# Optimization experiments

Measured on AMD Instinct MI355X. Metric: run time of the kernel, lower is better.

## Reference

```python
import jax, jax.numpy as jnp
import numpy as np

TEMPERATURE = 8.0  # sqrt(d_attn) with d_attn = 64
EPS = 1e-12


def _cv_softmax(z):
    """Complex softmax: softmax applied to magnitude, phase preserved.
    result = softmax(|z|, axis=-1) * z / |z|
    """
    mag = jnp.abs(z)                          # [B,H,S,S] real
    w = jax.nn.softmax(mag, axis=-1)          # softmax over magnitudes
    phase = z / jnp.maximum(mag, EPS)         # unit-modulus phase, guarded at 0
    return (w * phase).astype(z.dtype)


def setup_inputs() -> dict:
    key = jax.random.key(0)
    ks = jax.random.split(key, 6)
    shape = (4, 8, 2048, 64)  # [B, H, S, D]
    names = ["q_real", "q_imag", "k_real", "k_imag", "v_real", "v_imag"]
    return {n: jax.random.normal(k, shape, dtype=jnp.float32) for n, k in zip(names, ks)}


def reference(q_real, q_imag, k_real, k_imag, v_real, v_imag):
    q = jax.lax.complex(q_real, q_imag)
    k = jax.lax.complex(k_real, k_imag)
    v = jax.lax.complex(v_real, v_imag)
    # attn = (Q / t) K^T   (complex matmul)   [B,H,S,S]
    attn = jnp.einsum("bhsd,bhtd->bhst", q / TEMPERATURE, k)
    attn = _cv_softmax(attn)  # dropout is identity in eval mode
    out = jnp.einsum("bhst,bhtd->bhsd", attn, v)  # [B,H,S,D] complex
    # return as stacked real array [2, B, H, S, D] (real, imag)
    return jnp.stack([jnp.real(out), jnp.imag(out)], axis=0)
```

## Files before the change

### kernel.cpp

```cpp
#include <hip/hip_runtime.h>
#include <math.h>

typedef _Float16 half8   __attribute__((ext_vector_type(8)));
typedef _Float16 half4_t __attribute__((ext_vector_type(4)));
typedef float    floatx4 __attribute__((ext_vector_type(4)));

namespace {

constexpr int S  = 2048;
constexpr int D  = 64;
constexpr int BH = 32;
constexpr int QT = 64;
constexpr int KT = 64;
constexpr int STP = 72;
constexpr float INV_T = 0.125f;
constexpr size_t PLANE = (size_t)BH * S * D;
constexpr float MBIAS = 2.772588722239781f;

#define MFMA16(a, b, c) __builtin_amdgcn_mfma_f32_16x16x32_f16((a), (b), (c), 0, 0, 0)

typedef __attribute__((address_space(1))) const unsigned int guint;
typedef __attribute__((address_space(3))) unsigned int luint;

__device__ __forceinline__ void gl_lds16(const _Float16* g, _Float16* l) {
    __builtin_amdgcn_global_load_lds((guint*)g, (luint*)l, 16, 0, 0);
}

__global__ __launch_bounds__(256)
void prep_k(const float* __restrict__ kr, const float* __restrict__ ki,
            _Float16* __restrict__ okr, _Float16* __restrict__ oki)
{
    const float* src = blockIdx.z ? ki : kr;
    _Float16*    dst = blockIdx.z ? oki : okr;
    const int bh = (int)blockIdx.y, t0 = (int)blockIdx.x * 64;
    const int r  = (int)threadIdx.x >> 2, cg = (int)threadIdx.x & 3;
    const size_t in = ((size_t)bh * S + t0 + r) * D + cg * 16;
    float4 f0 = *(const float4*)(src + in);
    float4 f1 = *(const float4*)(src + in + 4);
    float4 f2 = *(const float4*)(src + in + 8);
    float4 f3 = *(const float4*)(src + in + 12);
    half8 h0, h1;
    h0[0]=(_Float16)f0.x; h0[1]=(_Float16)f0.y; h0[2]=(_Float16)f0.z; h0[3]=(_Float16)f0.w;
    h0[4]=(_Float16)f1.x; h0[5]=(_Float16)f1.y; h0[6]=(_Float16)f1.z; h0[7]=(_Float16)f1.w;
    h1[0]=(_Float16)f2.x; h1[1]=(_Float16)f2.y; h1[2]=(_Float16)f2.z; h1[3]=(_Float16)f2.w;
    h1[4]=(_Float16)f3.x; h1[5]=(_Float16)f3.y; h1[6]=(_Float16)f3.z; h1[7]=(_Float16)f3.w;
    const int key = r & 7;
    const size_t ob = ((size_t)bh * S + t0 + r) * D;
    *(half8*)(dst + ob + ((cg*2    ) ^ key) * 8) = h0;
    *(half8*)(dst + ob + ((cg*2 + 1) ^ key) * 8) = h1;
}

__global__ __launch_bounds__(256)
void prep_v(const float* __restrict__ vr, const float* __restrict__ vi,
            _Float16* __restrict__ ovr, _Float16* __restrict__ ovi)
{
    __shared__ _Float16 tile[64][72];
    const float* src = blockIdx.z ? vi : vr;
    _Float16*    dst = blockIdx.z ? ovi : ovr;
    const int bh = (int)blockIdx.y, t0 = (int)blockIdx.x * 64;
    const int r  = (int)threadIdx.x >> 2, cg = (int)threadIdx.x & 3;
    const size_t in = ((size_t)bh * S + t0 + r) * D + cg * 16;
    #pragma unroll
    for (int j = 0; j < 4; ++j) {
        float4 f = *(const float4*)(src + in + j * 4);
        tile[cg*16 + j*4 + 0][r] = (_Float16)f.x;
        tile[cg*16 + j*4 + 1][r] = (_Float16)f.y;
        tile[cg*16 + j*4 + 2][r] = (_Float16)f.z;
        tile[cg*16 + j*4 + 3][r] = (_Float16)f.w;
    }
    __syncthreads();
    const int d = r;
    const int key = d & 7;
    const size_t ob = ((size_t)bh * D + d) * S + t0;
    half8 a = *(const half8*)&tile[d][cg*16];
    half8 b = *(const half8*)&tile[d][cg*16 + 8];
    *(half8*)(dst + ob + ((cg*2    ) ^ key) * 8) = a;
    *(half8*)(dst + ob + ((cg*2 + 1) ^ key) * 8) = b;
}

__global__ __launch_bounds__(256, 3)
void cv_attn_f16(const float* __restrict__ qr_g, const float* __restrict__ qi_g,
                 const _Float16* __restrict__ kh_r, const _Float16* __restrict__ kh_i,
                 const _Float16* __restrict__ vt_r, const _Float16* __restrict__ vt_i,
                 float* __restrict__ out)
{
    __shared__ __align__(16) _Float16 sm[4*64*64 + 4*2*16*STP];
    _Float16* const Kr = sm;
    _Float16* const Ki = Kr + 64*64;
    _Float16* const Vr = Ki + 64*64;
    _Float16* const Vi = Vr + 64*64;
    _Float16* const Pb = Vi + 64*64;

    const int tid = (int)threadIdx.x, lane = tid & 63, wv = tid >> 6;
    const int g = lane >> 4, m = lane & 15;

    const int b   = (int)blockIdx.x;
    const int xcd = b & 7, y = b >> 3;
    const int qt  = y & 31, bh = xcd + 8 * (y >> 5);
    const int q0  = qt * QT;
    const size_t base = (size_t)bh * S * D;

    _Float16* const Pr = Pb + wv * (2*16*STP);
    _Float16* const Pi = Pr + 16*STP;

    const int ck0 = ((g    ) ^ (m & 7)) * 8;
    const int ck1 = ((g + 4) ^ (m & 7)) * 8;
    const int rb  = m * 64;
    const int pofs = m * STP + g * 8;

    half8 aqr[2], aqi[2], aqin[2];
    {
        const size_t qoff = base + (size_t)(q0 + wv*16 + m) * D + g*8;
        #pragma unroll
        for (int kc = 0; kc < 2; ++kc) {
            float4 r0 = *(const float4*)(qr_g + qoff + kc*32);
            float4 r1 = *(const float4*)(qr_g + qoff + kc*32 + 4);
            float4 i0 = *(const float4*)(qi_g + qoff + kc*32);
            float4 i1 = *(const float4*)(qi_g + qoff + kc*32 + 4);
            half8 hr, hi;
            hr[0]=(_Float16)(r0.x*INV_T); hr[1]=(_Float16)(r0.y*INV_T);
            hr[2]=(_Float16)(r0.z*INV_T); hr[3]=(_Float16)(r0.w*INV_T);
            hr[4]=(_Float16)(r1.x*INV_T); hr[5]=(_Float16)(r1.y*INV_T);
            hr[6]=(_Float16)(r1.z*INV_T); hr[7]=(_Float16)(r1.w*INV_T);
            hi[0]=(_Float16)(i0.x*INV_T); hi[1]=(_Float16)(i0.y*INV_T);
            hi[2]=(_Float16)(i0.z*INV_T); hi[3]=(_Float16)(i0.w*INV_T);
            hi[4]=(_Float16)(i1.x*INV_T); hi[5]=(_Float16)(i1.y*INV_T);
            hi[6]=(_Float16)(i1.z*INV_T); hi[7]=(_Float16)(i1.w*INV_T);
            aqr[kc] = hr; aqi[kc] = hi; aqin[kc] = -hi;
        }
    }

    floatx4 Or[4], Oi[4];
    float l_run[4] = {0.f, 0.f, 0.f, 0.f};
    #pragma unroll
    for (int nt = 0; nt < 4; ++nt) {
        Or[nt] = (floatx4){0.f,0.f,0.f,0.f};
        Oi[nt] = (floatx4){0.f,0.f,0.f,0.f};
    }

    for (int kt = 0; kt < S/KT; ++kt) {
        const int k0 = kt * KT;
        __syncthreads();

        if (wv < 2) {
            const _Float16* src = (wv ? kh_i : kh_r) + ((size_t)bh*S + k0)*D + lane*8;
            _Float16* dst = (wv ? Ki : Kr);
            #pragma unroll
            for (int i = 0; i < 8; ++i)
                gl_lds16(src + i*512, dst + i*512);
        } else {
            const _Float16* src = (wv == 2 ? vt_r : vt_i)
                                + ((size_t)bh*D + (lane>>3))*S + k0 + (lane&7)*8;
            _Float16* dst = (wv == 2 ? Vr : Vi);
            #pragma unroll
            for (int i = 0; i < 8; ++i)
                gl_lds16(src + (size_t)i*8*S, dst + i*512);
        }
        __syncthreads();

        floatx4 Zr[4], Zi[4];
        #pragma unroll
        for (int nt = 0; nt < 4; ++nt) {
            const int o = nt*16*64 + rb;
            half8 bkr0 = *(const half8*)&Kr[o + ck0];
            half8 bki0 = *(const half8*)&Ki[o + ck0];
            half8 bkr1 = *(const half8*)&Kr[o + ck1];
            half8 bki1 = *(const half8*)&Ki[o + ck1];
            floatx4 zr = (floatx4){0.f,0.f,0.f,0.f};
            floatx4 zi = (floatx4){0.f,0.f,0.f,0.f};
            zr = MFMA16(aqr[0],  bkr0, zr);
            zr = MFMA16(aqin[0], bki0, zr);
            zr = MFMA16(aqr[1],  bkr1, zr);
            zr = MFMA16(aqin[1], bki1, zr);
            zi = MFMA16(aqr[0],  bki0, zi);
            zi = MFMA16(aqi[0],  bkr0, zi);
            zi = MFMA16(aqr[1],  bki1, zi);
            zi = MFMA16(aqi[1],  bkr1, zi);
            Zr[nt] = zr; Zi[nt] = zi;
        }

        #pragma unroll
        for (int nt = 0; nt < 4; ++nt) {
            #pragma unroll
            for (int r = 0; r < 4; ++r) {
                const float zr = Zr[nt][r], zi = Zi[nt][r];
                const float s2  = fmaf(zr, zr, fmaf(zi, zi, 1e-24f));
                const float inv = __builtin_amdgcn_rsqf(s2);
                const float mag = s2 * inv;
                const float p   = __expf(mag - MBIAS);
                l_run[r] += p;
                const float w = p * inv;
                Pr[(4*g + r)*STP + nt*16 + m] = (_Float16)(w * zr);
                Pi[(4*g + r)*STP + nt*16 + m] = (_Float16)(w * zi);
            }
        }

        half8 apr[2], api[2], apin[2];
        apr[0] = *(const half8*)&Pr[pofs];      apr[1] = *(const half8*)&Pr[pofs + 32];
        api[0] = *(const half8*)&Pi[pofs];      api[1] = *(const half8*)&Pi[pofs + 32];
        apin[0] = -api[0]; apin[1] = -api[1];
        #pragma unroll
        for (int nt = 0; nt < 4; ++nt) {
            const int o = nt*16*64 + rb;
            half8 bvr0 = *(const half8*)&Vr[o + ck0];
            half8 bvi0 = *(const half8*)&Vi[o + ck0];
            half8 bvr1 = *(const half8*)&Vr[o + ck1];
            half8 bvi1 = *(const half8*)&Vi[o + ck1];
            floatx4 or_ = Or[nt], oi_ = Oi[nt];
            or_ = MFMA16(apr[0],  bvr0, or_);
            or_ = MFMA16(apin[0], bvi0, or_);
            or_ = MFMA16(apr[1],  bvr1, or_);
            or_ = MFMA16(apin[1], bvi1, or_);
            oi_ = MFMA16(apr[0],  bvi0, oi_);
            oi_ = MFMA16(api[0],  bvr0, oi_);
            oi_ = MFMA16(apr[1],  bvi1, oi_);
            oi_ = MFMA16(api[1],  bvr1, oi_);
            Or[nt] = or_; Oi[nt] = oi_;
        }
    }

    #pragma unroll
    for (int off = 1; off < 16; off <<= 1)
        #pragma unroll
        for (int r = 0; r < 4; ++r)
            l_run[r] += __shfl_xor(l_run[r], off, 64);

    #pragma unroll
    for (int r = 0; r < 4; ++r) {
        const float linv = 1.0f / l_run[r];
        const size_t o = base + (size_t)(q0 + wv*16 + 4*g + r) * D + m;
        #pragma unroll
        for (int nt = 0; nt < 4; ++nt) {
            out[o + nt*16]         = Or[nt][r] * linv;
            out[PLANE + o + nt*16] = Oi[nt][r] * linv;
        }
    }
}

constexpr int ST2 = 72;
__global__ __launch_bounds__(256, 2)
void cv_attn_mfma(const float* __restrict__ qr_g, const float* __restrict__ qi_g,
                  const float* __restrict__ kr_g, const float* __restrict__ ki_g,
                  const float* __restrict__ vr_g, const float* __restrict__ vi_g,
                  float* __restrict__ out)
{
    __shared__ __align__(16) _Float16 sm[4*64*ST2 + 4*2*16*ST2];
    _Float16* const Kr = sm;
    _Float16* const Ki = Kr + 64*ST2;
    _Float16* const Vr = Ki + 64*ST2;
    _Float16* const Vi = Vr + 64*ST2;
    _Float16* const Pb = Vi + 64*ST2;

    const int tid = (int)threadIdx.x, lane = tid & 63, wv = tid >> 6;
    const int g = lane >> 4, m = lane & 15;
    const int bh = (int)blockIdx.y;
    const int q0 = (int)blockIdx.x * QT;
    const size_t base = (size_t)bh * S * D;
    _Float16* const Pr = Pb + wv * (2*16*ST2);
    _Float16* const Pi = Pr + 16*ST2;
    const int lofs = m*ST2 + g*8;

    half8 aqr[2], aqi[2], aqin[2];
    {
        const size_t qoff = base + (size_t)(q0 + wv*16 + m) * D + g*8;
        #pragma unroll
        for (int kc = 0; kc < 2; ++kc) {
            float4 r0 = *(const float4*)(qr_g + qoff + kc*32);
            float4 r1 = *(const float4*)(qr_g + qoff + kc*32 + 4);
            float4 i0 = *(const float4*)(qi_g + qoff + kc*32);
            float4 i1 = *(const float4*)(qi_g + qoff + kc*32 + 4);
            half8 hr, hi;
            hr[0]=(_Float16)(r0.x*INV_T); hr[1]=(_Float16)(r0.y*INV_T);
            hr[2]=(_Float16)(r0.z*INV_T); hr[3]=(_Float16)(r0.w*INV_T);
            hr[4]=(_Float16)(r1.x*INV_T); hr[5]=(_Float16)(r1.y*INV_T);
            hr[6]=(_Float16)(r1.z*INV_T); hr[7]=(_Float16)(r1.w*INV_T);
            hi[0]=(_Float16)(i0.x*INV_T); hi[1]=(_Float16)(i0.y*INV_T);
            hi[2]=(_Float16)(i0.z*INV_T); hi[3]=(_Float16)(i0.w*INV_T);
            hi[4]=(_Float16)(i1.x*INV_T); hi[5]=(_Float16)(i1.y*INV_T);
            hi[6]=(_Float16)(i1.z*INV_T); hi[7]=(_Float16)(i1.w*INV_T);
            aqr[kc] = hr; aqi[kc] = hi; aqin[kc] = -hi;
        }
    }

    floatx4 Or[4], Oi[4];
    float m_run[4], l_run[4];
    #pragma unroll
    for (int r = 0; r < 4; ++r) { m_run[r] = -INFINITY; l_run[r] = 0.f; }
    #pragma unroll
    for (int nt = 0; nt < 4; ++nt) {
        Or[nt] = (floatx4){0.f,0.f,0.f,0.f};
        Oi[nt] = (floatx4){0.f,0.f,0.f,0.f};
    }

    for (int kt = 0; kt < S/KT; ++kt) {
        const int k0 = kt * KT;
        __syncthreads();
        if (wv < 2) {
            const float* src = (wv == 0 ? kr_g : ki_g) + base + (size_t)k0 * D;
            _Float16* dst = (wv == 0 ? Kr : Ki);
            #pragma unroll
            for (int it = 0; it < 16; ++it) {
                const int e = it*64 + lane, t = e >> 4, c4 = (e & 15) * 4;
                float4 v = *(const float4*)(src + t*64 + c4);
                half4_t h = {(_Float16)v.x, (_Float16)v.y, (_Float16)v.z, (_Float16)v.w};
                *(half4_t*)&dst[t*ST2 + c4] = h;
            }
        } else {
            const float* src = (wv == 2 ? vr_g : vi_g) + base + (size_t)k0 * D;
            _Float16* dst = (wv == 2 ? Vr : Vi);
            #pragma unroll
            for (int t0 = 0; t0 < KT; t0 += 4) {
                float v0 = src[(t0+0)*64 + lane];
                float v1 = src[(t0+1)*64 + lane];
                float v2 = src[(t0+2)*64 + lane];
                float v3 = src[(t0+3)*64 + lane];
                half4_t h = {(_Float16)v0, (_Float16)v1, (_Float16)v2, (_Float16)v3};
                *(half4_t*)&dst[lane*ST2 + t0] = h;
            }
        }
        __syncthreads();

        floatx4 Zr[4], Zi[4];
        #pragma unroll
        for (int nt = 0; nt < 4; ++nt) {
            floatx4 zr = (floatx4){0.f,0.f,0.f,0.f};
            floatx4 zi = (floatx4){0.f,0.f,0.f,0.f};
            #pragma unroll
            for (int kc = 0; kc < 2; ++kc) {
                const int o = nt*16*ST2 + lofs + kc*32;
                half8 bkr = *(const half8*)&Kr[o];
                half8 bki = *(const half8*)&Ki[o];
                zr = MFMA16(aqr[kc],  bkr, zr);
                zr = MFMA16(aqin[kc], bki, zr);
                zi = MFMA16(aqr[kc],  bki, zi);
                zi = MFMA16(aqi[kc],  bkr, zi);
            }
            Zr[nt] = zr; Zi[nt] = zi;
        }

        float mag[4][4], mt[4] = {0.f,0.f,0.f,0.f};
        #pragma unroll
        for (int nt = 0; nt < 4; ++nt)
            #pragma unroll
            for (int r = 0; r < 4; ++r) {
                const float a = Zr[nt][r], bz = Zi[nt][r];
                const float s = __builtin_amdgcn_sqrtf(a*a + bz*bz);
                mag[nt][r] = s; mt[r] = fmaxf(mt[r], s);
            }
        #pragma unroll
        for (int off = 1; off < 16; off <<= 1)
            #pragma unroll
            for (int r = 0; r < 4; ++r)
                mt[r] = fmaxf(mt[r], __shfl_xor(mt[r], off, 64));

        float alpha[4], rs[4];
        #pragma unroll
        for (int r = 0; r < 4; ++r) {
            const float mnew = fmaxf(m_run[r], mt[r]);
            alpha[r] = __expf(m_run[r] - mnew);
            m_run[r] = mnew; rs[r] = 0.f;
        }
        #pragma unroll
        for (int nt = 0; nt < 4; ++nt)
            #pragma unroll
            for (int r = 0; r < 4; ++r) {
                const float p = __expf(mag[nt][r] - m_run[r]);
                rs[r] += p;
                const float w = p * __builtin_amdgcn_rcpf(fmaxf(mag[nt][r], 1e-12f));
                Pr[(4*g + r)*ST2 + nt*16 + m] = (_Float16)(w * Zr[nt][r]);
                Pi[(4*g + r)*ST2 + nt*16 + m] = (_Float16)(w * Zi[nt][r]);
            }
        #pragma unroll
        for (int off = 1; off < 16; off <<= 1)
            #pragma unroll
            for (int r = 0; r < 4; ++r)
                rs[r] += __shfl_xor(rs[r], off, 64);
        #pragma unroll
        for (int r = 0; r < 4; ++r) l_run[r] = l_run[r]*alpha[r] + rs[r];

        #pragma unroll
        for (int nt = 0; nt < 4; ++nt)
            #pragma unroll
            for (int r = 0; r < 4; ++r) { Or[nt][r] *= alpha[r]; Oi[nt][r] *= alpha[r]; }

        half8 apr[2], api[2], apin[2];
        #pragma unroll
        for (int kc = 0; kc < 2; ++kc) {
            apr[kc]  = *(const half8*)&Pr[lofs + kc*32];
            api[kc]  = *(const half8*)&Pi[lofs + kc*32];
            apin[kc] = -api[kc];
        }
        #pragma unroll
        for (int nt = 0; nt < 4; ++nt) {
            floatx4 ors = Or[nt], ois = Oi[nt];
            #pragma unroll
            for (int kc = 0; kc < 2; ++kc) {
                const int o = nt*16*ST2 + lofs + kc*32;
                half8 bvr = *(const half8*)&Vr[o];
                half8 bvi = *(const half8*)&Vi[o];
                ors = MFMA16(apr[kc],  bvr, ors);
                ors = MFMA16(apin[kc], bvi, ors);
                ois = MFMA16(apr[kc],  bvi, ois);
                ois = MFMA16(api[kc],  bvr, ois);
            }
            Or[nt] = ors; Oi[nt] = ois;
        }
    }

    #pragma unroll
    for (int r = 0; r < 4; ++r) {
        const float linv = 1.0f / l_run[r];
        const size_t o = base + (size_t)(q0 + wv*16 + 4*g + r) * D + m;
        #pragma unroll
        for (int nt = 0; nt < 4; ++nt) {
            out[o + nt*16]         = Or[nt][r] * linv;
            out[PLANE + o + nt*16] = Oi[nt][r] * linv;
        }
    }
}

}

extern "C" void kernel_launch(void* const* d_in, const int* in_sizes, int n_in,
                              void* d_out, int out_size, void* d_ws, size_t ws_size,
                              hipStream_t stream) {
    const float* qr = (const float*)d_in[0];
    const float* qi = (const float*)d_in[1];
    const float* kr = (const float*)d_in[2];
    const float* ki = (const float*)d_in[3];
    const float* vr = (const float*)d_in[4];
    const float* vi = (const float*)d_in[5];
    float* out = (float*)d_out;

    const size_t PH = (size_t)BH * S * D;
    const size_t need = 4 * PH * sizeof(_Float16);
    if (ws_size >= need) {
        _Float16* khr = (_Float16*)d_ws;
        _Float16* khi = khr + PH;
        _Float16* vtr = khi + PH;
        _Float16* vti = vtr + PH;
        prep_k<<<dim3(32, 32, 2), 256, 0, stream>>>(kr, ki, khr, khi);
        prep_v<<<dim3(32, 32, 2), 256, 0, stream>>>(vr, vi, vtr, vti);
        cv_attn_f16<<<1024, 256, 0, stream>>>(qr, qi, khr, khi, vtr, vti, out);
    } else {
        cv_attn_mfma<<<dim3(32, 32), 256, 0, stream>>>(qr, qi, kr, ki, vr, vi, out);
    }
}
```

Baseline: 314.8 us.

## Switch attention to 32x32 MFMA with split-key waves and fuse prep kernels

Replaces the 16x16x32 MFMA attention kernel with a 32x32x16 variant. Each wave now covers a 32-query by 32-key quadrant, two waves split the keys of each 64-key tile, and their partial outputs and row sums are combined through LDS at the end. The two K and V prep kernels are merged into one launch with a 4-deep grid z dimension. The goal is fewer MFMA issues and LDS fragment reads per tile, and one less launch. In exchange the kernel holds larger accumulators (fewer blocks per CU under launch_bounds 2), does an extra LDS reduction, and negates K on every iteration.

```diff
diff --git a/kernel.cpp b/kernel.cpp
--- a/kernel.cpp
+++ b/kernel.cpp
@@ -3,7 +3,8 @@
 
 typedef _Float16 half8   __attribute__((ext_vector_type(8)));
 typedef _Float16 half4_t __attribute__((ext_vector_type(4)));
-typedef float    floatx4 __attribute__((ext_vector_type(4)));
+typedef float    floatx4  __attribute__((ext_vector_type(4)));
+typedef float    floatx16 __attribute__((ext_vector_type(16)));
 
 namespace {
 
@@ -12,11 +13,12 @@
 constexpr int BH = 32;
 constexpr int QT = 64;
 constexpr int KT = 64;
-constexpr int STP = 72;
+constexpr int PST = 40;
 constexpr float INV_T = 0.125f;
 constexpr size_t PLANE = (size_t)BH * S * D;
 constexpr float MBIAS = 2.772588722239781f;
 
+#define MFMA32(a, b, c) __builtin_amdgcn_mfma_f32_32x32x16_f16((a), (b), (c), 0, 0, 0)
 #define MFMA16(a, b, c) __builtin_amdgcn_mfma_f32_16x16x32_f16((a), (b), (c), 0, 0, 0)
 
 typedef __attribute__((address_space(1))) const unsigned int guint;
@@ -27,64 +29,65 @@
 }
 
 __global__ __launch_bounds__(256)
-void prep_k(const float* __restrict__ kr, const float* __restrict__ ki,
-            _Float16* __restrict__ okr, _Float16* __restrict__ oki)
-{
-    const float* src = blockIdx.z ? ki : kr;
-    _Float16*    dst = blockIdx.z ? oki : okr;
-    const int bh = (int)blockIdx.y, t0 = (int)blockIdx.x * 64;
-    const int r  = (int)threadIdx.x >> 2, cg = (int)threadIdx.x & 3;
-    const size_t in = ((size_t)bh * S + t0 + r) * D + cg * 16;
-    float4 f0 = *(const float4*)(src + in);
-    float4 f1 = *(const float4*)(src + in + 4);
-    float4 f2 = *(const float4*)(src + in + 8);
-    float4 f3 = *(const float4*)(src + in + 12);
-    half8 h0, h1;
-    h0[0]=(_Float16)f0.x; h0[1]=(_Float16)f0.y; h0[2]=(_Float16)f0.z; h0[3]=(_Float16)f0.w;
-    h0[4]=(_Float16)f1.x; h0[5]=(_Float16)f1.y; h0[6]=(_Float16)f1.z; h0[7]=(_Float16)f1.w;
-    h1[0]=(_Float16)f2.x; h1[1]=(_Float16)f2.y; h1[2]=(_Float16)f2.z; h1[3]=(_Float16)f2.w;
-    h1[4]=(_Float16)f3.x; h1[5]=(_Float16)f3.y; h1[6]=(_Float16)f3.z; h1[7]=(_Float16)f3.w;
-    const int key = r & 7;
-    const size_t ob = ((size_t)bh * S + t0 + r) * D;
-    *(half8*)(dst + ob + ((cg*2    ) ^ key) * 8) = h0;
-    *(half8*)(dst + ob + ((cg*2 + 1) ^ key) * 8) = h1;
-}
-
-__global__ __launch_bounds__(256)
-void prep_v(const float* __restrict__ vr, const float* __restrict__ vi,
-            _Float16* __restrict__ ovr, _Float16* __restrict__ ovi)
+void prep_all(const float* __restrict__ kr, const float* __restrict__ ki,
+              const float* __restrict__ vr, const float* __restrict__ vi,
+              _Float16* __restrict__ okr, _Float16* __restrict__ oki,
+              _Float16* __restrict__ ovr, _Float16* __restrict__ ovi)
 {
     __shared__ _Float16 tile[64][72];
-    const float* src = blockIdx.z ? vi : vr;
-    _Float16*    dst = blockIdx.z ? ovi : ovr;
+    const int z  = (int)blockIdx.z;
     const int bh = (int)blockIdx.y, t0 = (int)blockIdx.x * 64;
-    const int r  = (int)threadIdx.x >> 2, cg = (int)threadIdx.x & 3;
-    const size_t in = ((size_t)bh * S + t0 + r) * D + cg * 16;
-    #pragma unroll
-    for (int j = 0; j < 4; ++j) {
-        float4 f = *(const float4*)(src + in + j * 4);
-        tile[cg*16 + j*4 + 0][r] = (_Float16)f.x;
-        tile[cg*16 + j*4 + 1][r] = (_Float16)f.y;
-        tile[cg*16 + j*4 + 2][r] = (_Float16)f.z;
-        tile[cg*16 + j*4 + 3][r] = (_Float16)f.w;
-    }
-    __syncthreads();
-    const int d = r;
-    const int key = d & 7;
-    const size_t ob = ((size_t)bh * D + d) * S + t0;
-    half8 a = *(const half8*)&tile[d][cg*16];
-    half8 b = *(const half8*)&tile[d][cg*16 + 8];
-    *(half8*)(dst + ob + ((cg*2    ) ^ key) * 8) = a;
-    *(half8*)(dst + ob + ((cg*2 + 1) ^ key) * 8) = b;
-}
-
-__global__ __launch_bounds__(256, 3)
-void cv_attn_f16(const float* __restrict__ qr_g, const float* __restrict__ qi_g,
-                 const _Float16* __restrict__ kh_r, const _Float16* __restrict__ kh_i,
-                 const _Float16* __restrict__ vt_r, const _Float16* __restrict__ vt_i,
-                 float* __restrict__ out)
+    const int tid = (int)threadIdx.x;
+
+    if (z < 2) {
+        const float* src = z ? ki : kr;
+        _Float16*    dst = z ? oki : okr;
+        const int r = tid >> 2, cg = tid & 3;
+        const size_t in = ((size_t)bh * S + t0 + r) * D + cg * 16;
+        float4 f0 = *(const float4*)(src + in);
+        float4 f1 = *(const float4*)(src + in + 4);
+        float4 f2 = *(const float4*)(src + in + 8);
+        float4 f3 = *(const float4*)(src + in + 12);
+        half8 h0, h1;
+        h0[0]=(_Float16)f0.x; h0[1]=(_Float16)f0.y; h0[2]=(_Float16)f0.z; h0[3]=(_Float16)f0.w;
+        h0[4]=(_Float16)f1.x; h0[5]=(_Float16)f1.y; h0[6]=(_Float16)f1.z; h0[7]=(_Float16)f1.w;
+        h1[0]=(_Float16)f2.x; h1[1]=(_Float16)f2.y; h1[2]=(_Float16)f2.z; h1[3]=(_Float16)f2.w;
+        h1[4]=(_Float16)f3.x; h1[5]=(_Float16)f3.y; h1[6]=(_Float16)f3.z; h1[7]=(_Float16)f3.w;
+        const int key = r & 7;
+        const size_t ob = ((size_t)bh * S + t0 + r) * D;
+        *(half8*)(dst + ob + ((cg*2    ) ^ key) * 8) = h0;
+        *(half8*)(dst + ob + ((cg*2 + 1) ^ key) * 8) = h1;
+    } else {
+        const float* src = (z == 3) ? vi : vr;
+        _Float16*    dst = (z == 3) ? ovi : ovr;
+        const int r = tid & 63, cg = tid >> 6;
+        const size_t in = ((size_t)bh * S + t0 + r) * D + cg * 16;
+        #pragma unroll
+        for (int j = 0; j < 4; ++j) {
+            float4 f = *(const float4*)(src + in + j * 4);
+            tile[cg*16 + j*4 + 0][r] = (_Float16)f.x;
+            tile[cg*16 + j*4 + 1][r] = (_Float16)f.y;
+            tile[cg*16 + j*4 + 2][r] = (_Float16)f.z;
+            tile[cg*16 + j*4 + 3][r] = (_Float16)f.w;
+        }
+        __syncthreads();
+        const int d = tid >> 2, c2 = tid & 3;
+        const int key = d & 7;
+        const size_t ob = ((size_t)bh * D + d) * S + t0;
+        half8 a = *(const half8*)&tile[d][c2*16];
+        half8 b = *(const half8*)&tile[d][c2*16 + 8];
+        *(half8*)(dst + ob + ((c2*2    ) ^ key) * 8) = a;
+        *(half8*)(dst + ob + ((c2*2 + 1) ^ key) * 8) = b;
+    }
+}
+
+__global__ __launch_bounds__(256, 2)
+void cv_attn_3232(const float* __restrict__ qr_g, const float* __restrict__ qi_g,
+                  const _Float16* __restrict__ kh_r, const _Float16* __restrict__ kh_i,
+                  const _Float16* __restrict__ vt_r, const _Float16* __restrict__ vt_i,
+                  float* __restrict__ out)
 {
-    __shared__ __align__(16) _Float16 sm[4*64*64 + 4*2*16*STP];
+    __shared__ __align__(16) _Float16 sm[4*64*64 + 4*2*32*PST];
     _Float16* const Kr = sm;
     _Float16* const Ki = Kr + 64*64;
     _Float16* const Vr = Ki + 64*64;
@@ -92,7 +95,8 @@
     _Float16* const Pb = Vi + 64*64;
 
     const int tid = (int)threadIdx.x, lane = tid & 63, wv = tid >> 6;
-    const int g = lane >> 4, m = lane & 15;
+    const int qh = wv & 1, th = wv >> 1;
+    const int l5 = lane & 31, h = lane >> 5;
 
     const int b   = (int)blockIdx.x;
     const int xcd = b & 7, y = b >> 3;
@@ -100,13 +104,179 @@
     const int q0  = qt * QT;
     const size_t base = (size_t)bh * S * D;
 
-    _Float16* const Pr = Pb + wv * (2*16*STP);
-    _Float16* const Pi = Pr + 16*STP;
-
-    const int ck0 = ((g    ) ^ (m & 7)) * 8;
-    const int ck1 = ((g + 4) ^ (m & 7)) * 8;
-    const int rb  = m * 64;
-    const int pofs = m * STP + g * 8;
+    _Float16* const Pr = Pb + wv * (2*32*PST);
+    _Float16* const Pi = Pr + 32*PST;
+
+    half8 aqr[4], aqi[4];
+    {
+        const size_t qoff = base + (size_t)(q0 + qh*32 + l5) * D + h*8;
+        #pragma unroll
+        for (int c = 0; c < 4; ++c) {
+            float4 r0 = *(const float4*)(qr_g + qoff + c*16);
+            float4 r1 = *(const float4*)(qr_g + qoff + c*16 + 4);
+            float4 i0 = *(const float4*)(qi_g + qoff + c*16);
+            float4 i1 = *(const float4*)(qi_g + qoff + c*16 + 4);
+            half8 hr, hi;
+            hr[0]=(_Float16)(r0.x*INV_T); hr[1]=(_Float16)(r0.y*INV_T);
+            hr[2]=(_Float16)(r0.z*INV_T); hr[3]=(_Float16)(r0.w*INV_T);
+            hr[4]=(_Float16)(r1.x*INV_T); hr[5]=(_Float16)(r1.y*INV_T);
+            hr[6]=(_Float16)(r1.z*INV_T); hr[7]=(_Float16)(r1.w*INV_T);
+            hi[0]=(_Float16)(i0.x*INV_T); hi[1]=(_Float16)(i0.y*INV_T);
+            hi[2]=(_Float16)(i0.z*INV_T); hi[3]=(_Float16)(i0.w*INV_T);
+            hi[4]=(_Float16)(i1.x*INV_T); hi[5]=(_Float16)(i1.y*INV_T);
+            hi[6]=(_Float16)(i1.z*INV_T); hi[7]=(_Float16)(i1.w*INV_T);
+            aqr[c] = hr; aqi[c] = hi;
+        }
+    }
+
+    floatx16 Or[2], Oi[2];
+    float l_run[16];
+    #pragma unroll
+    for (int r = 0; r < 16; ++r) l_run[r] = 0.f;
+    #pragma unroll
+    for (int dt = 0; dt < 2; ++dt) {
+        #pragma unroll
+        for (int r = 0; r < 16; ++r) { Or[dt][r] = 0.f; Oi[dt][r] = 0.f; }
+    }
+
+    const int krow  = th*32 + l5;
+    const int kbase = krow * 64;
+    const int kkey  = l5 & 7;
+
+    for (int kt = 0; kt < S/KT; ++kt) {
+        const int k0 = kt * KT;
+        __syncthreads();
+
+        if (wv < 2) {
+            const _Float16* src = (wv ? kh_i : kh_r) + ((size_t)bh*S + k0)*D + lane*8;
+            _Float16* dst = (wv ? Ki : Kr);
+            #pragma unroll
+            for (int i = 0; i < 8; ++i)
+                gl_lds16(src + i*512, dst + i*512);
+        } else {
+            const _Float16* src = (wv == 2 ? vt_r : vt_i)
+                                + ((size_t)bh*D + (lane>>3))*S + k0 + (lane&7)*8;
+            _Float16* dst = (wv == 2 ? Vr : Vi);
+            #pragma unroll
+            for (int i = 0; i < 8; ++i)
+                gl_lds16(src + (size_t)i*8*S, dst + i*512);
+        }
+        __syncthreads();
+
+        floatx16 Zr, Zi;
+        #pragma unroll
+        for (int r = 0; r < 16; ++r) { Zr[r] = 0.f; Zi[r] = 0.f; }
+        #pragma unroll
+        for (int c = 0; c < 4; ++c) {
+            const int ck = (((c<<1) | h) ^ kkey) << 3;
+            half8 bkr = *(const half8*)&Kr[kbase + ck];
+            half8 bki = *(const half8*)&Ki[kbase + ck];
+            half8 nki = -bki;
+            Zr = MFMA32(aqr[c], bkr, Zr);
+            Zr = MFMA32(aqi[c], nki, Zr);
+            Zi = MFMA32(aqr[c], bki, Zi);
+            Zi = MFMA32(aqi[c], bkr, Zi);
+        }
+
+        #pragma unroll
+        for (int r = 0; r < 16; ++r) {
+            const float zr = Zr[r], zi = Zi[r];
+            const float s2  = fmaf(zr, zr, fmaf(zi, zi, 1e-24f));
+            const float inv = __builtin_amdgcn_rsqf(s2);
+            const float mag = s2 * inv;
+            const float p   = __expf(mag - MBIAS);
+            l_run[r] += p;
+            const float w = p * inv;
+            const int qrow = (r & 3) + 8*(r >> 2) + 4*h;
+            Pr[qrow*PST + l5] = (_Float16)(w * zr);
+            Pi[qrow*PST + l5] = (_Float16)(w * zi);
+        }
+
+        #pragma unroll
+        for (int c2 = 0; c2 < 2; ++c2) {
+            const int po = l5*PST + c2*16 + h*8;
+            half8 apr = *(const half8*)&Pr[po];
+            half8 api = *(const half8*)&Pi[po];
+            half8 nai = -api;
+            #pragma unroll
+            for (int dt = 0; dt < 2; ++dt) {
+                const int vbase = (dt*32 + l5) * 64;
+                const int vck = ((th*4 + c2*2 + h) ^ kkey) << 3;
+                half8 bvr = *(const half8*)&Vr[vbase + vck];
+                half8 bvi = *(const half8*)&Vi[vbase + vck];
+                Or[dt] = MFMA32(apr, bvr, Or[dt]);
+                Or[dt] = MFMA32(nai, bvi, Or[dt]);
+                Oi[dt] = MFMA32(apr, bvi, Oi[dt]);
+                Oi[dt] = MFMA32(api, bvr, Oi[dt]);
+            }
+        }
+    }
+
+    __syncthreads();
+    float* const red = (float*)sm;
+    if (th == 1) {
+        float* dst = red + qh * 5120;
+        #pragma unroll
+        for (int r = 0; r < 16; ++r) {
+            dst[(r     )*64 + lane] = Or[0][r];
+            dst[(r + 16)*64 + lane] = Or[1][r];
+            dst[(r + 32)*64 + lane] = Oi[0][r];
+            dst[(r + 48)*64 + lane] = Oi[1][r];
+            dst[(r + 64)*64 + lane] = l_run[r];
+        }
+    }
+    __syncthreads();
+    if (th == 0) {
+        const float* src2 = red + qh * 5120;
+        #pragma unroll
+        for (int r = 0; r < 16; ++r) {
+            Or[0][r] += src2[(r     )*64 + lane];
+            Or[1][r] += src2[(r + 16)*64 + lane];
+            Oi[0][r] += src2[(r + 32)*64 + lane];
+            Oi[1][r] += src2[(r + 48)*64 + lane];
+            l_run[r] += src2[(r + 64)*64 + lane];
+        }
+        #pragma unroll
+        for (int off = 1; off < 32; off <<= 1)
+            #pragma unroll
+            for (int r = 0; r < 16; ++r)
+                l_run[r] += __shfl_xor(l_run[r], off, 64);
+
+        #pragma unroll
+        for (int r = 0; r < 16; ++r) {
+            const float linv = 1.0f / l_run[r];
+            const int qrow = (r & 3) + 8*(r >> 2) + 4*h;
+            const size_t o = base + (size_t)(q0 + qh*32 + qrow) * D + l5;
+            out[o]              = Or[0][r] * linv;
+            out[o + 32]         = Or[1][r] * linv;
+            out[PLANE + o]      = Oi[0][r] * linv;
+            out[PLANE + o + 32] = Oi[1][r] * linv;
+        }
+    }
+}
+
+constexpr int ST2 = 72;
+__global__ __launch_bounds__(256, 2)
+void cv_attn_mfma(const float* __restrict__ qr_g, const float* __restrict__ qi_g,
+                  const float* __restrict__ kr_g, const float* __restrict__ ki_g,
+                  const float* __restrict__ vr_g, const float* __restrict__ vi_g,
+                  float* __restrict__ out)
+{
+    __shared__ __align__(16) _Float16 sm[4*64*ST2 + 4*2*16*ST2];
+    _Float16* const Kr = sm;
+    _Float16* const Ki = Kr + 64*ST2;
+    _Float16* const Vr = Ki + 64*ST2;
+    _Float16* const Vi = Vr + 64*ST2;
+    _Float16* const Pb = Vi + 64*ST2;
+
+    const int tid = (int)threadIdx.x, lane = tid & 63, wv = tid >> 6;
+    const int g = lane >> 4, m = lane & 15;
+    const int bh = (int)blockIdx.y;
+    const int q0 = (int)blockIdx.x * QT;
+    const size_t base = (size_t)bh * S * D;
+    _Float16* const Pr = Pb + wv * (2*16*ST2);
+    _Float16* const Pi = Pr + 16*ST2;
+    const int lofs = m*ST2 + g*8;
 
     half8 aqr[2], aqi[2], aqin[2];
     {
@@ -131,158 +301,6 @@
     }
 
     floatx4 Or[4], Oi[4];
-    float l_run[4] = {0.f, 0.f, 0.f, 0.f};
-    #pragma unroll
-    for (int nt = 0; nt < 4; ++nt) {
-        Or[nt] = (floatx4){0.f,0.f,0.f,0.f};
-        Oi[nt] = (floatx4){0.f,0.f,0.f,0.f};
-    }
-
-    for (int kt = 0; kt < S/KT; ++kt) {
-        const int k0 = kt * KT;
-        __syncthreads();
-
-        if (wv < 2) {
-            const _Float16* src = (wv ? kh_i : kh_r) + ((size_t)bh*S + k0)*D + lane*8;
-            _Float16* dst = (wv ? Ki : Kr);
-            #pragma unroll
-            for (int i = 0; i < 8; ++i)
-                gl_lds16(src + i*512, dst + i*512);
-        } else {
-            const _Float16* src = (wv == 2 ? vt_r : vt_i)
-                                + ((size_t)bh*D + (lane>>3))*S + k0 + (lane&7)*8;
-            _Float16* dst = (wv == 2 ? Vr : Vi);
-            #pragma unroll
-            for (int i = 0; i < 8; ++i)
-                gl_lds16(src + (size_t)i*8*S, dst + i*512);
-        }
-        __syncthreads();
-
-        floatx4 Zr[4], Zi[4];
-        #pragma unroll
-        for (int nt = 0; nt < 4; ++nt) {
-            const int o = nt*16*64 + rb;
-            half8 bkr0 = *(const half8*)&Kr[o + ck0];
-            half8 bki0 = *(const half8*)&Ki[o + ck0];
-            half8 bkr1 = *(const half8*)&Kr[o + ck1];
-            half8 bki1 = *(const half8*)&Ki[o + ck1];
-            floatx4 zr = (floatx4){0.f,0.f,0.f,0.f};
-            floatx4 zi = (floatx4){0.f,0.f,0.f,0.f};
-            zr = MFMA16(aqr[0],  bkr0, zr);
-            zr = MFMA16(aqin[0], bki0, zr);
-            zr = MFMA16(aqr[1],  bkr1, zr);
-            zr = MFMA16(aqin[1], bki1, zr);
-            zi = MFMA16(aqr[0],  bki0, zi);
-            zi = MFMA16(aqi[0],  bkr0, zi);
-            zi = MFMA16(aqr[1],  bki1, zi);
-            zi = MFMA16(aqi[1],  bkr1, zi);
-            Zr[nt] = zr; Zi[nt] = zi;
-        }
-
-        #pragma unroll
-        for (int nt = 0; nt < 4; ++nt) {
-            #pragma unroll
-            for (int r = 0; r < 4; ++r) {
-                const float zr = Zr[nt][r], zi = Zi[nt][r];
-                const float s2  = fmaf(zr, zr, fmaf(zi, zi, 1e-24f));
-                const float inv = __builtin_amdgcn_rsqf(s2);
-                const float mag = s2 * inv;
-                const float p   = __expf(mag - MBIAS);
-                l_run[r] += p;
-                const float w = p * inv;
-                Pr[(4*g + r)*STP + nt*16 + m] = (_Float16)(w * zr);
-                Pi[(4*g + r)*STP + nt*16 + m] = (_Float16)(w * zi);
-            }
-        }
-
-        half8 apr[2], api[2], apin[2];
-        apr[0] = *(const half8*)&Pr[pofs];      apr[1] = *(const half8*)&Pr[pofs + 32];
-        api[0] = *(const half8*)&Pi[pofs];      api[1] = *(const half8*)&Pi[pofs + 32];
-        apin[0] = -api[0]; apin[1] = -api[1];
-        #pragma unroll
-        for (int nt = 0; nt < 4; ++nt) {
-            const int o = nt*16*64 + rb;
-            half8 bvr0 = *(const half8*)&Vr[o + ck0];
-            half8 bvi0 = *(const half8*)&Vi[o + ck0];
-            half8 bvr1 = *(const half8*)&Vr[o + ck1];
-            half8 bvi1 = *(const half8*)&Vi[o + ck1];
-            floatx4 or_ = Or[nt], oi_ = Oi[nt];
-            or_ = MFMA16(apr[0],  bvr0, or_);
-            or_ = MFMA16(apin[0], bvi0, or_);
-            or_ = MFMA16(apr[1],  bvr1, or_);
-            or_ = MFMA16(apin[1], bvi1, or_);
-            oi_ = MFMA16(apr[0],  bvi0, oi_);
-            oi_ = MFMA16(api[0],  bvr0, oi_);
-            oi_ = MFMA16(apr[1],  bvi1, oi_);
-            oi_ = MFMA16(api[1],  bvr1, oi_);
-            Or[nt] = or_; Oi[nt] = oi_;
-        }
-    }
-
-    #pragma unroll
-    for (int off = 1; off < 16; off <<= 1)
-        #pragma unroll
-        for (int r = 0; r < 4; ++r)
-            l_run[r] += __shfl_xor(l_run[r], off, 64);
-
-    #pragma unroll
-    for (int r = 0; r < 4; ++r) {
-        const float linv = 1.0f / l_run[r];
-        const size_t o = base + (size_t)(q0 + wv*16 + 4*g + r) * D + m;
-        #pragma unroll
-        for (int nt = 0; nt < 4; ++nt) {
-            out[o + nt*16]         = Or[nt][r] * linv;
-            out[PLANE + o + nt*16] = Oi[nt][r] * linv;
-        }
-    }
-}
-
-constexpr int ST2 = 72;
-__global__ __launch_bounds__(256, 2)
-void cv_attn_mfma(const float* __restrict__ qr_g, const float* __restrict__ qi_g,
-                  const float* __restrict__ kr_g, const float* __restrict__ ki_g,
-                  const float* __restrict__ vr_g, const float* __restrict__ vi_g,
-                  float* __restrict__ out)
-{
-    __shared__ __align__(16) _Float16 sm[4*64*ST2 + 4*2*16*ST2];
-    _Float16* const Kr = sm;
-    _Float16* const Ki = Kr + 64*ST2;
-    _Float16* const Vr = Ki + 64*ST2;
-    _Float16* const Vi = Vr + 64*ST2;
-    _Float16* const Pb = Vi + 64*ST2;
-
-    const int tid = (int)threadIdx.x, lane = tid & 63, wv = tid >> 6;
-    const int g = lane >> 4, m = lane & 15;
-    const int bh = (int)blockIdx.y;
-    const int q0 = (int)blockIdx.x * QT;
-    const size_t base = (size_t)bh * S * D;
-    _Float16* const Pr = Pb + wv * (2*16*ST2);
-    _Float16* const Pi = Pr + 16*ST2;
-    const int lofs = m*ST2 + g*8;
-
-    half8 aqr[2], aqi[2], aqin[2];
-    {
-        const size_t qoff = base + (size_t)(q0 + wv*16 + m) * D + g*8;
-        #pragma unroll
-        for (int kc = 0; kc < 2; ++kc) {
-            float4 r0 = *(const float4*)(qr_g + qoff + kc*32);
-            float4 r1 = *(const float4*)(qr_g + qoff + kc*32 + 4);
-            float4 i0 = *(const float4*)(qi_g + qoff + kc*32);
-            float4 i1 = *(const float4*)(qi_g + qoff + kc*32 + 4);
-            half8 hr, hi;
-            hr[0]=(_Float16)(r0.x*INV_T); hr[1]=(_Float16)(r0.y*INV_T);
-            hr[2]=(_Float16)(r0.z*INV_T); hr[3]=(_Float16)(r0.w*INV_T);
-            hr[4]=(_Float16)(r1.x*INV_T); hr[5]=(_Float16)(r1.y*INV_T);
-            hr[6]=(_Float16)(r1.z*INV_T); hr[7]=(_Float16)(r1.w*INV_T);
-            hi[0]=(_Float16)(i0.x*INV_T); hi[1]=(_Float16)(i0.y*INV_T);
-            hi[2]=(_Float16)(i0.z*INV_T); hi[3]=(_Float16)(i0.w*INV_T);
-            hi[4]=(_Float16)(i1.x*INV_T); hi[5]=(_Float16)(i1.y*INV_T);
-            hi[6]=(_Float16)(i1.z*INV_T); hi[7]=(_Float16)(i1.w*INV_T);
-            aqr[kc] = hr; aqi[kc] = hi; aqin[kc] = -hi;
-        }
-    }
-
-    floatx4 Or[4], Oi[4];
     float m_run[4], l_run[4];
     #pragma unroll
     for (int r = 0; r < 4; ++r) { m_run[r] = -INFINITY; l_run[r] = 0.f; }
@@ -302,8 +320,8 @@
             for (int it = 0; it < 16; ++it) {
                 const int e = it*64 + lane, t = e >> 4, c4 = (e & 15) * 4;
                 float4 v = *(const float4*)(src + t*64 + c4);
-                half4_t h = {(_Float16)v.x, (_Float16)v.y, (_Float16)v.z, (_Float16)v.w};
-                *(half4_t*)&dst[t*ST2 + c4] = h;
+                half4_t hh = {(_Float16)v.x, (_Float16)v.y, (_Float16)v.z, (_Float16)v.w};
+                *(half4_t*)&dst[t*ST2 + c4] = hh;
             }
         } else {
             const float* src = (wv == 2 ? vr_g : vi_g) + base + (size_t)k0 * D;
@@ -314,8 +332,8 @@
                 float v1 = src[(t0+1)*64 + lane];
                 float v2 = src[(t0+2)*64 + lane];
                 float v3 = src[(t0+3)*64 + lane];
-                half4_t h = {(_Float16)v0, (_Float16)v1, (_Float16)v2, (_Float16)v3};
-                *(half4_t*)&dst[lane*ST2 + t0] = h;
+                half4_t hh = {(_Float16)v0, (_Float16)v1, (_Float16)v2, (_Float16)v3};
+                *(half4_t*)&dst[lane*ST2 + t0] = hh;
             }
         }
         __syncthreads();
@@ -439,9 +457,8 @@
         _Float16* khi = khr + PH;
         _Float16* vtr = khi + PH;
         _Float16* vti = vtr + PH;
-        prep_k<<<dim3(32, 32, 2), 256, 0, stream>>>(kr, ki, khr, khi);
-        prep_v<<<dim3(32, 32, 2), 256, 0, stream>>>(vr, vi, vtr, vti);
-        cv_attn_f16<<<1024, 256, 0, stream>>>(qr, qi, khr, khi, vtr, vti, out);
+        prep_all<<<dim3(32, 32, 4), 256, 0, stream>>>(kr, ki, vr, vi, khr, khi, vtr, vti);
+        cv_attn_3232<<<1024, 256, 0, stream>>>(qr, qi, khr, khi, vtr, vti, out);
     } else {
         cv_attn_mfma<<<dim3(32, 32), 256, 0, stream>>>(qr, qi, kr, ki, vr, vi, out);
     }
```

After: 322.9 us. 1.03x slower.

## Double-buffer K/V tiles with 32-key steps and merge prep kernels

Applied to the files above, without the earlier changes.

The attention kernel now stages K and V in 32-key tiles into two LDS buffers, so the async global-to-LDS loads for the next tile overlap compute on the current one. This replaces the previous load-sync-compute loop with its two barriers per 64-key tile. The K and V prep kernels are merged into one launch, and the V transpose uses a new 4-way swizzle to match the 32-wide tile. Smaller tiles mean more barriers and fewer MFMAs per sync, and the swizzle change must stay consistent between the prep and attention kernels.

```diff
diff --git a/kernel.cpp b/kernel.cpp
--- a/kernel.cpp
+++ b/kernel.cpp
@@ -11,8 +11,7 @@
 constexpr int D  = 64;
 constexpr int BH = 32;
 constexpr int QT = 64;
-constexpr int KT = 64;
-constexpr int STP = 72;
+constexpr int PST = 40;
 constexpr float INV_T = 0.125f;
 constexpr size_t PLANE = (size_t)BH * S * D;
 constexpr float MBIAS = 2.772588722239781f;
@@ -27,69 +26,67 @@
 }
 
 __global__ __launch_bounds__(256)
-void prep_k(const float* __restrict__ kr, const float* __restrict__ ki,
-            _Float16* __restrict__ okr, _Float16* __restrict__ oki)
-{
-    const float* src = blockIdx.z ? ki : kr;
-    _Float16*    dst = blockIdx.z ? oki : okr;
-    const int bh = (int)blockIdx.y, t0 = (int)blockIdx.x * 64;
-    const int r  = (int)threadIdx.x >> 2, cg = (int)threadIdx.x & 3;
-    const size_t in = ((size_t)bh * S + t0 + r) * D + cg * 16;
-    float4 f0 = *(const float4*)(src + in);
-    float4 f1 = *(const float4*)(src + in + 4);
-    float4 f2 = *(const float4*)(src + in + 8);
-    float4 f3 = *(const float4*)(src + in + 12);
-    half8 h0, h1;
-    h0[0]=(_Float16)f0.x; h0[1]=(_Float16)f0.y; h0[2]=(_Float16)f0.z; h0[3]=(_Float16)f0.w;
-    h0[4]=(_Float16)f1.x; h0[5]=(_Float16)f1.y; h0[6]=(_Float16)f1.z; h0[7]=(_Float16)f1.w;
-    h1[0]=(_Float16)f2.x; h1[1]=(_Float16)f2.y; h1[2]=(_Float16)f2.z; h1[3]=(_Float16)f2.w;
-    h1[4]=(_Float16)f3.x; h1[5]=(_Float16)f3.y; h1[6]=(_Float16)f3.z; h1[7]=(_Float16)f3.w;
-    const int key = r & 7;
-    const size_t ob = ((size_t)bh * S + t0 + r) * D;
-    *(half8*)(dst + ob + ((cg*2    ) ^ key) * 8) = h0;
-    *(half8*)(dst + ob + ((cg*2 + 1) ^ key) * 8) = h1;
-}
-
-__global__ __launch_bounds__(256)
-void prep_v(const float* __restrict__ vr, const float* __restrict__ vi,
-            _Float16* __restrict__ ovr, _Float16* __restrict__ ovi)
+void prep_all(const float* __restrict__ kr, const float* __restrict__ ki,
+              const float* __restrict__ vr, const float* __restrict__ vi,
+              _Float16* __restrict__ okr, _Float16* __restrict__ oki,
+              _Float16* __restrict__ ovr, _Float16* __restrict__ ovi)
 {
     __shared__ _Float16 tile[64][72];
-    const float* src = blockIdx.z ? vi : vr;
-    _Float16*    dst = blockIdx.z ? ovi : ovr;
+    const int z  = (int)blockIdx.z;
     const int bh = (int)blockIdx.y, t0 = (int)blockIdx.x * 64;
-    const int r  = (int)threadIdx.x >> 2, cg = (int)threadIdx.x & 3;
-    const size_t in = ((size_t)bh * S + t0 + r) * D + cg * 16;
-    #pragma unroll
-    for (int j = 0; j < 4; ++j) {
-        float4 f = *(const float4*)(src + in + j * 4);
-        tile[cg*16 + j*4 + 0][r] = (_Float16)f.x;
-        tile[cg*16 + j*4 + 1][r] = (_Float16)f.y;
-        tile[cg*16 + j*4 + 2][r] = (_Float16)f.z;
-        tile[cg*16 + j*4 + 3][r] = (_Float16)f.w;
-    }
-    __syncthreads();
-    const int d = r;
-    const int key = d & 7;
-    const size_t ob = ((size_t)bh * D + d) * S + t0;
-    half8 a = *(const half8*)&tile[d][cg*16];
-    half8 b = *(const half8*)&tile[d][cg*16 + 8];
-    *(half8*)(dst + ob + ((cg*2    ) ^ key) * 8) = a;
-    *(half8*)(dst + ob + ((cg*2 + 1) ^ key) * 8) = b;
+    const int tid = (int)threadIdx.x;
+
+    if (z < 2) {
+        const float* src = z ? ki : kr;
+        _Float16*    dst = z ? oki : okr;
+        const int r = tid >> 2, cg = tid & 3;
+        const size_t in = ((size_t)bh * S + t0 + r) * D + cg * 16;
+        float4 f0 = *(const float4*)(src + in);
+        float4 f1 = *(const float4*)(src + in + 4);
+        float4 f2 = *(const float4*)(src + in + 8);
+        float4 f3 = *(const float4*)(src + in + 12);
+        half8 h0, h1;
+        h0[0]=(_Float16)f0.x; h0[1]=(_Float16)f0.y; h0[2]=(_Float16)f0.z; h0[3]=(_Float16)f0.w;
+        h0[4]=(_Float16)f1.x; h0[5]=(_Float16)f1.y; h0[6]=(_Float16)f1.z; h0[7]=(_Float16)f1.w;
+        h1[0]=(_Float16)f2.x; h1[1]=(_Float16)f2.y; h1[2]=(_Float16)f2.z; h1[3]=(_Float16)f2.w;
+        h1[4]=(_Float16)f3.x; h1[5]=(_Float16)f3.y; h1[6]=(_Float16)f3.z; h1[7]=(_Float16)f3.w;
+        const int key = r & 7;
+        const size_t ob = ((size_t)bh * S + t0 + r) * D;
+        *(half8*)(dst + ob + ((cg*2    ) ^ key) * 8) = h0;
+        *(half8*)(dst + ob + ((cg*2 + 1) ^ key) * 8) = h1;
+    } else {
+        const float* src = (z == 3) ? vi : vr;
+        _Float16*    dst = (z == 3) ? ovi : ovr;
+        const int r = tid & 63, cg = tid >> 6;
+        const size_t in = ((size_t)bh * S + t0 + r) * D + cg * 16;
+        #pragma unroll
+        for (int j = 0; j < 4; ++j) {
+            float4 f = *(const float4*)(src + in + j * 4);
+            tile[cg*16 + j*4 + 0][r] = (_Float16)f.x;
+            tile[cg*16 + j*4 + 1][r] = (_Float16)f.y;
+            tile[cg*16 + j*4 + 2][r] = (_Float16)f.z;
+            tile[cg*16 + j*4 + 3][r] = (_Float16)f.w;
+        }
+        __syncthreads();
+        const int d = tid >> 2, c2 = tid & 3;
+        const int key = d & 3;
+        const size_t ob = ((size_t)bh * D + d) * S + t0;
+        half8 a = *(const half8*)&tile[d][c2*16];
+        half8 b = *(const half8*)&tile[d][c2*16 + 8];
+        const int j0 = c2*2, j1 = c2*2 + 1;
+        *(half8*)(dst + ob + (size_t)(((j0 & 4) | ((j0 & 3) ^ key))) * 8) = a;
+        *(half8*)(dst + ob + (size_t)(((j1 & 4) | ((j1 & 3) ^ key))) * 8) = b;
+    }
 }
 
 __global__ __launch_bounds__(256, 3)
-void cv_attn_f16(const float* __restrict__ qr_g, const float* __restrict__ qi_g,
-                 const _Float16* __restrict__ kh_r, const _Float16* __restrict__ kh_i,
-                 const _Float16* __restrict__ vt_r, const _Float16* __restrict__ vt_i,
-                 float* __restrict__ out)
+void cv_attn_db(const float* __restrict__ qr_g, const float* __restrict__ qi_g,
+                const _Float16* __restrict__ kh_r, const _Float16* __restrict__ kh_i,
+                const _Float16* __restrict__ vt_r, const _Float16* __restrict__ vt_i,
+                float* __restrict__ out)
 {
-    __shared__ __align__(16) _Float16 sm[4*64*64 + 4*2*16*STP];
-    _Float16* const Kr = sm;
-    _Float16* const Ki = Kr + 64*64;
-    _Float16* const Vr = Ki + 64*64;
-    _Float16* const Vi = Vr + 64*64;
-    _Float16* const Pb = Vi + 64*64;
+    __shared__ __align__(16) _Float16 sm[2*4*2048 + 4*2*16*PST];
+    _Float16* const Pb = sm + 2*4*2048;
 
     const int tid = (int)threadIdx.x, lane = tid & 63, wv = tid >> 6;
     const int g = lane >> 4, m = lane & 15;
@@ -100,13 +97,8 @@
     const int q0  = qt * QT;
     const size_t base = (size_t)bh * S * D;
 
-    _Float16* const Pr = Pb + wv * (2*16*STP);
-    _Float16* const Pi = Pr + 16*STP;
-
-    const int ck0 = ((g    ) ^ (m & 7)) * 8;
-    const int ck1 = ((g + 4) ^ (m & 7)) * 8;
-    const int rb  = m * 64;
-    const int pofs = m * STP + g * 8;
+    _Float16* const Pr = Pb + wv * (2*16*PST);
+    _Float16* const Pi = Pr + 16*PST;
 
     half8 aqr[2], aqi[2], aqin[2];
     {
@@ -138,34 +130,40 @@
         Oi[nt] = (floatx4){0.f,0.f,0.f,0.f};
     }
 
-    for (int kt = 0; kt < S/KT; ++kt) {
-        const int k0 = kt * KT;
-        __syncthreads();
-
+    auto stage = [&](int kt, _Float16* bs) {
+        const int k0 = kt * 32;
         if (wv < 2) {
             const _Float16* src = (wv ? kh_i : kh_r) + ((size_t)bh*S + k0)*D + lane*8;
-            _Float16* dst = (wv ? Ki : Kr);
-            #pragma unroll
-            for (int i = 0; i < 8; ++i)
+            _Float16* dst = bs + wv*2048;
+            #pragma unroll
+            for (int i = 0; i < 4; ++i)
                 gl_lds16(src + i*512, dst + i*512);
         } else {
             const _Float16* src = (wv == 2 ? vt_r : vt_i)
-                                + ((size_t)bh*D + (lane>>3))*S + k0 + (lane&7)*8;
-            _Float16* dst = (wv == 2 ? Vr : Vi);
-            #pragma unroll
-            for (int i = 0; i < 8; ++i)
-                gl_lds16(src + (size_t)i*8*S, dst + i*512);
-        }
-        __syncthreads();
-
-        floatx4 Zr[4], Zi[4];
-        #pragma unroll
-        for (int nt = 0; nt < 4; ++nt) {
-            const int o = nt*16*64 + rb;
-            half8 bkr0 = *(const half8*)&Kr[o + ck0];
-            half8 bki0 = *(const half8*)&Ki[o + ck0];
-            half8 bkr1 = *(const half8*)&Kr[o + ck1];
-            half8 bki1 = *(const half8*)&Ki[o + ck1];
+                                + ((size_t)bh*D + (lane>>2))*S + k0 + (lane&3)*8;
+            _Float16* dst = bs + wv*2048;
+            #pragma unroll
+            for (int i = 0; i < 4; ++i)
+                gl_lds16(src + (size_t)i*16*S, dst + i*512);
+        }
+    };
+
+    auto compute = [&](_Float16* bs) {
+        _Float16* const Krt = bs;
+        _Float16* const Kit = bs + 2048;
+        _Float16* const Vrt = bs + 4096;
+        _Float16* const Vit = bs + 6144;
+
+        floatx4 Zr[2], Zi[2];
+        #pragma unroll
+        for (int nt = 0; nt < 2; ++nt) {
+            const int rb  = (nt*16 + m) * 64;
+            const int key = m & 7;
+            const int ck0 = (g ^ key) * 8, ck1 = ((g + 4) ^ key) * 8;
+            half8 bkr0 = *(const half8*)&Krt[rb + ck0];
+            half8 bki0 = *(const half8*)&Kit[rb + ck0];
+            half8 bkr1 = *(const half8*)&Krt[rb + ck1];
+            half8 bki1 = *(const half8*)&Kit[rb + ck1];
             floatx4 zr = (floatx4){0.f,0.f,0.f,0.f};
             floatx4 zi = (floatx4){0.f,0.f,0.f,0.f};
             zr = MFMA16(aqr[0],  bkr0, zr);
@@ -180,7 +178,7 @@
         }
 
         #pragma unroll
-        for (int nt = 0; nt < 4; ++nt) {
+        for (int nt = 0; nt < 2; ++nt) {
             #pragma unroll
             for (int r = 0; r < 4; ++r) {
                 const float zr = Zr[nt][r], zi = Zi[nt][r];
@@ -190,33 +188,38 @@
                 const float p   = __expf(mag - MBIAS);
                 l_run[r] += p;
                 const float w = p * inv;
-                Pr[(4*g + r)*STP + nt*16 + m] = (_Float16)(w * zr);
-                Pi[(4*g + r)*STP + nt*16 + m] = (_Float16)(w * zi);
-            }
-        }
-
-        half8 apr[2], api[2], apin[2];
-        apr[0] = *(const half8*)&Pr[pofs];      apr[1] = *(const half8*)&Pr[pofs + 32];
-        api[0] = *(const half8*)&Pi[pofs];      api[1] = *(const half8*)&Pi[pofs + 32];
-        apin[0] = -api[0]; apin[1] = -api[1];
+                Pr[(4*g + r)*PST + nt*16 + m] = (_Float16)(w * zr);
+                Pi[(4*g + r)*PST + nt*16 + m] = (_Float16)(w * zi);
+            }
+        }
+
+        half8 apr = *(const half8*)&Pr[m*PST + g*8];
+        half8 api = *(const half8*)&Pi[m*PST + g*8];
+        half8 nai = -api;
         #pragma unroll
         for (int nt = 0; nt < 4; ++nt) {
-            const int o = nt*16*64 + rb;
-            half8 bvr0 = *(const half8*)&Vr[o + ck0];
-            half8 bvi0 = *(const half8*)&Vi[o + ck0];
-            half8 bvr1 = *(const half8*)&Vr[o + ck1];
-            half8 bvi1 = *(const half8*)&Vi[o + ck1];
-            floatx4 or_ = Or[nt], oi_ = Oi[nt];
-            or_ = MFMA16(apr[0],  bvr0, or_);
-            or_ = MFMA16(apin[0], bvi0, or_);
-            or_ = MFMA16(apr[1],  bvr1, or_);
-            or_ = MFMA16(apin[1], bvi1, or_);
-            oi_ = MFMA16(apr[0],  bvi0, oi_);
-            oi_ = MFMA16(api[0],  bvr0, oi_);
-            oi_ = MFMA16(apr[1],  bvi1, oi_);
-            oi_ = MFMA16(api[1],  bvr1, oi_);
-            Or[nt] = or_; Oi[nt] = oi_;
-        }
+            const int vrb = (nt*16 + m) * 32;
+            const int vck = (g ^ (m & 3)) * 8;
+            half8 bvr = *(const half8*)&Vrt[vrb + vck];
+            half8 bvi = *(const half8*)&Vit[vrb + vck];
+            Or[nt] = MFMA16(apr, bvr, Or[nt]);
+            Or[nt] = MFMA16(nai, bvi, Or[nt]);
+            Oi[nt] = MFMA16(apr, bvi, Oi[nt]);
+            Oi[nt] = MFMA16(api, bvr, Oi[nt]);
+        }
+    };
+
+    _Float16* const buf0 = sm;
+    _Float16* const buf1 = sm + 4*2048;
+
+    stage(0, buf0);
+    for (int kt = 0; kt < 64; kt += 2) {
+        __syncthreads();
+        stage(kt + 1, buf1);
+        compute(buf0);
+        __syncthreads();
+        if (kt < 62) stage(kt + 2, buf0);
+        compute(buf1);
     }
 
     #pragma unroll
@@ -292,8 +295,8 @@
         Oi[nt] = (floatx4){0.f,0.f,0.f,0.f};
     }
 
-    for (int kt = 0; kt < S/KT; ++kt) {
-        const int k0 = kt * KT;
+    for (int kt = 0; kt < S/64; ++kt) {
+        const int k0 = kt * 64;
         __syncthreads();
         if (wv < 2) {
             const float* src = (wv == 0 ? kr_g : ki_g) + base + (size_t)k0 * D;
@@ -302,20 +305,20 @@
             for (int it = 0; it < 16; ++it) {
                 const int e = it*64 + lane, t = e >> 4, c4 = (e & 15) * 4;
                 float4 v = *(const float4*)(src + t*64 + c4);
-                half4_t h = {(_Float16)v.x, (_Float16)v.y, (_Float16)v.z, (_Float16)v.w};
-                *(half4_t*)&dst[t*ST2 + c4] = h;
+                half4_t hh = {(_Float16)v.x, (_Float16)v.y, (_Float16)v.z, (_Float16)v.w};
+                *(half4_t*)&dst[t*ST2 + c4] = hh;
             }
         } else {
             const float* src = (wv == 2 ? vr_g : vi_g) + base + (size_t)k0 * D;
             _Float16* dst = (wv == 2 ? Vr : Vi);
             #pragma unroll
-            for (int t0 = 0; t0 < KT; t0 += 4) {
+            for (int t0 = 0; t0 < 64; t0 += 4) {
                 float v0 = src[(t0+0)*64 + lane];
                 float v1 = src[(t0+1)*64 + lane];
                 float v2 = src[(t0+2)*64 + lane];
                 float v3 = src[(t0+3)*64 + lane];
-                half4_t h = {(_Float16)v0, (_Float16)v1, (_Float16)v2, (_Float16)v3};
-                *(half4_t*)&dst[lane*ST2 + t0] = h;
+                half4_t hh = {(_Float16)v0, (_Float16)v1, (_Float16)v2, (_Float16)v3};
+                *(half4_t*)&dst[lane*ST2 + t0] = hh;
             }
         }
         __syncthreads();
@@ -439,9 +442,8 @@
         _Float16* khi = khr + PH;
         _Float16* vtr = khi + PH;
         _Float16* vti = vtr + PH;
-        prep_k<<<dim3(32, 32, 2), 256, 0, stream>>>(kr, ki, khr, khi);
-        prep_v<<<dim3(32, 32, 2), 256, 0, stream>>>(vr, vi, vtr, vti);
-        cv_attn_f16<<<1024, 256, 0, stream>>>(qr, qi, khr, khi, vtr, vti, out);
+        prep_all<<<dim3(32, 32, 4), 256, 0, stream>>>(kr, ki, vr, vi, khr, khi, vtr, vti);
+        cv_attn_db<<<1024, 256, 0, stream>>>(qr, qi, khr, khi, vtr, vti, out);
     } else {
         cv_attn_mfma<<<dim3(32, 32), 256, 0, stream>>>(qr, qi, kr, ki, vr, vi, out);
     }
```

Measured after the change: 301.7 us. -4.2%, faster.
